# Kernel tuning notes

Measured on AMD Instinct MI355X. Metric: run time of the kernel, lower is better.

The kernel has to match this reference:

```python
import jax, jax.numpy as jnp
import numpy as np

N_ATOMS = 8192
N_BONDS = 8192
N_ANGLES = 16384
N_DIHEDRALS = 24576


def _chain_idx(key, n, arity):
    # base atom index + consecutive offsets -> guaranteed-distinct atoms per interaction
    base = jax.random.randint(key, (n, 1), 0, N_ATOMS - arity, dtype=jnp.int32)
    return base + jnp.arange(arity, dtype=jnp.int32)[None, :]


def setup_inputs() -> dict:
    key = jax.random.key(0)
    ks = jax.random.split(key, 12)
    positions = jax.random.normal(ks[0], (N_ATOMS, 3), dtype=jnp.float32) * 3.0
    # LJ pair params: strictly-upper-triangular like the original __init__ loops
    triu = jnp.triu(jnp.ones((N_ATOMS, N_ATOMS), dtype=jnp.float32), k=1)
    sigma = jax.random.uniform(ks[1], (N_ATOMS, N_ATOMS), dtype=jnp.float32) * triu
    epsilon = jax.random.uniform(ks[2], (N_ATOMS, N_ATOMS), dtype=jnp.float32) * 0.2 * triu
    bond_idx = _chain_idx(ks[3], N_BONDS, 2)
    k_bond = jax.random.uniform(ks[4], (N_BONDS,), dtype=jnp.float32) * 300.0 + 100.0
    r0 = jax.random.uniform(ks[5], (N_BONDS,), dtype=jnp.float32) + 1.0
    angle_idx = _chain_idx(ks[6], N_ANGLES, 3)
    k_angle = jax.random.uniform(ks[7], (N_ANGLES,), dtype=jnp.float32) * 50.0 + 10.0
    theta0 = jax.random.uniform(ks[8], (N_ANGLES,), dtype=jnp.float32) * 2.0 + 0.5
    dihedral_idx = _chain_idx(ks[9], N_DIHEDRALS, 4)
    k_dihedral = jax.random.uniform(ks[10], (N_DIHEDRALS,), dtype=jnp.float32) * 5.0
    default_phase = jax.random.uniform(ks[11], (N_DIHEDRALS,), dtype=jnp.float32) * np.pi
    n_mult = jax.random.randint(jax.random.fold_in(key, 99), (N_DIHEDRALS,), 1, 4).astype(jnp.float32)
    return {
        "positions": positions,
        "sigma": sigma,
        "epsilon": epsilon,
        "k_bond": k_bond,
        "r0": r0,
        "bond_idx": bond_idx,
        "k_angle": k_angle,
        "theta0": theta0,
        "angle_idx": angle_idx,
        "k_dihedral": k_dihedral,
        "default_phase": default_phase,
        "n_mult": n_mult,
        "dihedral_idx": dihedral_idx,
    }


def _energy(positions, sigma, epsilon, k_bond, r0, bond_idx,
            k_angle, theta0, angle_idx, k_dihedral, default_phase, n_mult, dihedral_idx):
    # pairwise distance map (cdist) + 1e-9, as in get_distance_map
    sq = jnp.sum(positions * positions, axis=-1)  # [N]
    d2 = sq[:, None] + sq[None, :] - 2.0 * (positions @ positions.T)
    dist = jnp.sqrt(jnp.maximum(d2, 0.0)) + 1e-9  # [N, N]

    # bonds: gather pair distances, harmonic energy
    bd = dist[bond_idx[:, 0], bond_idx[:, 1]]
    bond_e = jnp.sum(0.5 * k_bond * (bd - r0) ** 2)

    # angles: acos of normalized dot product
    p1 = positions[angle_idx[:, 0]]
    p2 = positions[angle_idx[:, 1]]
    p3 = positions[angle_idx[:, 2]]
    v1 = p2 - p1
    v2 = p2 - p3
    cos_a = jnp.sum(v1 * v2, axis=-1) / (
        jnp.linalg.norm(v1, axis=1) * jnp.linalg.norm(v2, axis=1))
    ang = jnp.arccos(cos_a)
    angle_e = jnp.sum(0.5 * k_angle * (ang - theta0) ** 2)

    # dihedrals (faithful to the original formulas, including its denominators)
    q1 = positions[dihedral_idx[:, 0]]
    q2 = positions[dihedral_idx[:, 1]]
    q3 = positions[dihedral_idx[:, 2]]
    q4 = positions[dihedral_idx[:, 3]]
    w1 = q2 - q1
    w2 = q3 - q2
    w3 = q4 - q3
    n1 = jnp.cross(w1, w2)
    n2 = jnp.cross(w2, w3)
    cos_d = jnp.sum(n1 * n2, axis=-1) / (
        jnp.linalg.norm(w1, axis=1) * jnp.linalg.norm(w2, axis=1))
    sin_d = jnp.sum(jnp.cross(n1, n2) * w2, axis=-1) / (
        jnp.linalg.norm(w2, axis=1) * jnp.linalg.norm(n1, axis=1) * jnp.linalg.norm(n2, axis=1))
    dih = jnp.arctan2(sin_d, cos_d)
    dihedral_e = jnp.sum(0.5 * k_dihedral * (1.0 + jnp.cos(n_mult * dih - default_phase)))

    # Lennard-Jones over dense NxN pair matrices
    r6 = (sigma / dist) ** 6
    r12 = r6 * r6
    lj_e = jnp.sum(4.0 * epsilon * (r12 - r6))

    # NOTE: original forward computes coulomb but does NOT add it to total_energy
    return bond_e + angle_e + dihedral_e + lj_e


def reference(positions, sigma, epsilon, k_bond, r0, bond_idx,
              k_angle, theta0, angle_idx, k_dihedral, default_phase, n_mult, dihedral_idx):
    return _energy(positions, sigma, epsilon, k_bond, r0, bond_idx,
                   k_angle, theta0, angle_idx, k_dihedral, default_phase, n_mult, dihedral_idx)
```

## Files before the change

kernel.cpp:

```cpp
#include <hip/hip_runtime.h>

#define NATOMS   8192
#define NVEC     (NATOMS / 4)
#define BT       256
#define NB_LJ    NATOMS
#define NBONDS   8192
#define NANGLES  16384
#define NDIH     24576
#define NB_BOND  ((NBONDS + NANGLES + NDIH) / BT)

__device__ __forceinline__ float sq_np(float x, float y, float z)
{
    return __fadd_rn(__fadd_rn(__fmul_rn(x, x), __fmul_rn(y, y)),
                     __fmul_rn(z, z));
}

__global__ __launch_bounds__(BT)
void lj_kernel(const float* __restrict__ pos,
               const float* __restrict__ sigma,
               const float* __restrict__ eps,
               float* __restrict__ partial)
{
    const int i   = blockIdx.x;
    const int tid = threadIdx.x;

    const float xi = pos[3 * i + 0];
    const float yi = pos[3 * i + 1];
    const float zi = pos[3 * i + 2];
    const float sqi = sq_np(xi, yi, zi);

    const float* __restrict__ srow = sigma + (size_t)i * NATOMS;
    const float* __restrict__ erow = eps   + (size_t)i * NATOMS;

    float acc = 0.0f;
    const int v0 = (i + 1) >> 2;

    for (int v = v0 + tid; v < NVEC; v += BT) {
        const float4 s4 = *reinterpret_cast<const float4*>(srow + 4 * v);
        const float4 e4 = *reinterpret_cast<const float4*>(erow + 4 * v);
        const float4 p0 = *reinterpret_cast<const float4*>(pos + 12 * v + 0);
        const float4 p1 = *reinterpret_cast<const float4*>(pos + 12 * v + 4);
        const float4 p2 = *reinterpret_cast<const float4*>(pos + 12 * v + 8);

        const float px[4] = { p0.x, p0.w, p1.z, p2.y };
        const float py[4] = { p0.y, p1.x, p1.w, p2.z };
        const float pz[4] = { p0.z, p1.y, p2.x, p2.w };
        const float ss[4] = { s4.x, s4.y, s4.z, s4.w };
        const float ee[4] = { e4.x, e4.y, e4.z, e4.w };

        #pragma unroll
        for (int k = 0; k < 4; ++k) {
            float t = __fmul_rn(xi, px[k]);
            t = fmaf(yi, py[k], t);
            t = fmaf(zi, pz[k], t);
            const float sqj = sq_np(px[k], py[k], pz[k]);
            const float d2  = __fsub_rn(__fadd_rn(sqi, sqj),
                                        __fmul_rn(2.0f, t));
            const float dist  = __fadd_rn(__fsqrt_rn(fmaxf(d2, 0.0f)), 1e-9f);
            const float ratio = __fdiv_rn(ss[k], dist);
            const float r2  = __fmul_rn(ratio, ratio);
            const float r6  = __fmul_rn(__fmul_rn(r2, r2), r2);
            const float r12 = __fmul_rn(r6, r6);
            acc += 4.0f * ee[k] * (r12 - r6);
        }
    }

    #pragma unroll
    for (int off = 32; off > 0; off >>= 1)
        acc += __shfl_down(acc, off, 64);
    __shared__ float red[BT / 64];
    if ((tid & 63) == 0) red[tid >> 6] = acc;
    __syncthreads();
    if (tid == 0)
        partial[i] = red[0] + red[1] + red[2] + red[3];
}

__global__ __launch_bounds__(BT)
void bonded_kernel(const float* __restrict__ pos,
                   const float* __restrict__ k_bond,
                   const float* __restrict__ r0,
                   const int*   __restrict__ bidx,
                   const float* __restrict__ k_angle,
                   const float* __restrict__ th0,
                   const int*   __restrict__ aidx,
                   const float* __restrict__ k_dih,
                   const float* __restrict__ phase,
                   const float* __restrict__ nmult,
                   const int*   __restrict__ didx,
                   float* __restrict__ partial)
{
    const int t = blockIdx.x * BT + threadIdx.x;
    float e = 0.0f;

    if (t < NBONDS) {
        const int a = bidx[2 * t + 0];
        const int b = bidx[2 * t + 1];
        const float xa = pos[3 * a + 0], ya = pos[3 * a + 1], za = pos[3 * a + 2];
        const float xb = pos[3 * b + 0], yb = pos[3 * b + 1], zb = pos[3 * b + 2];
        float dt2 = __fmul_rn(xa, xb);
        dt2 = fmaf(ya, yb, dt2);
        dt2 = fmaf(za, zb, dt2);
        const float d2 = __fsub_rn(__fadd_rn(sq_np(xa, ya, za), sq_np(xb, yb, zb)),
                                   __fmul_rn(2.0f, dt2));
        const float d  = __fadd_rn(__fsqrt_rn(fmaxf(d2, 0.0f)), 1e-9f);
        const float dd = d - r0[t];
        e = 0.5f * k_bond[t] * dd * dd;
    } else if (t < NBONDS + NANGLES) {
        const int u = t - NBONDS;
        const int a = aidx[3 * u + 0];
        const int b = aidx[3 * u + 1];
        const int c = aidx[3 * u + 2];
        const float v1x = pos[3 * b + 0] - pos[3 * a + 0];
        const float v1y = pos[3 * b + 1] - pos[3 * a + 1];
        const float v1z = pos[3 * b + 2] - pos[3 * a + 2];
        const float v2x = pos[3 * b + 0] - pos[3 * c + 0];
        const float v2y = pos[3 * b + 1] - pos[3 * c + 1];
        const float v2z = pos[3 * b + 2] - pos[3 * c + 2];
        const float dot = fmaf(v1x, v2x, fmaf(v1y, v2y, v1z * v2z));
        const float n1  = sqrtf(fmaf(v1x, v1x, fmaf(v1y, v1y, v1z * v1z)));
        const float n2  = sqrtf(fmaf(v2x, v2x, fmaf(v2y, v2y, v2z * v2z)));
        float ca = dot / (n1 * n2);
        ca = fminf(1.0f, fmaxf(-1.0f, ca));
        const float ang = acosf(ca);
        const float dth = ang - th0[u];
        e = 0.5f * k_angle[u] * dth * dth;
    } else {
        const int u = t - NBONDS - NANGLES;
        const int a = didx[4 * u + 0];
        const int b = didx[4 * u + 1];
        const int c = didx[4 * u + 2];
        const int d = didx[4 * u + 3];
        const float w1x = pos[3 * b + 0] - pos[3 * a + 0];
        const float w1y = pos[3 * b + 1] - pos[3 * a + 1];
        const float w1z = pos[3 * b + 2] - pos[3 * a + 2];
        const float w2x = pos[3 * c + 0] - pos[3 * b + 0];
        const float w2y = pos[3 * c + 1] - pos[3 * b + 1];
        const float w2z = pos[3 * c + 2] - pos[3 * b + 2];
        const float w3x = pos[3 * d + 0] - pos[3 * c + 0];
        const float w3y = pos[3 * d + 1] - pos[3 * c + 1];
        const float w3z = pos[3 * d + 2] - pos[3 * c + 2];
        const float n1x = w1y * w2z - w1z * w2y;
        const float n1y = w1z * w2x - w1x * w2z;
        const float n1z = w1x * w2y - w1y * w2x;
        const float n2x = w2y * w3z - w2z * w3y;
        const float n2y = w2z * w3x - w2x * w3z;
        const float n2z = w2x * w3y - w2y * w3x;
        const float dot12 = fmaf(n1x, n2x, fmaf(n1y, n2y, n1z * n2z));
        const float nw1 = sqrtf(fmaf(w1x, w1x, fmaf(w1y, w1y, w1z * w1z)));
        const float nw2 = sqrtf(fmaf(w2x, w2x, fmaf(w2y, w2y, w2z * w2z)));
        const float nn1 = sqrtf(fmaf(n1x, n1x, fmaf(n1y, n1y, n1z * n1z)));
        const float nn2 = sqrtf(fmaf(n2x, n2x, fmaf(n2y, n2y, n2z * n2z)));
        const float cos_d = dot12 / (nw1 * nw2);
        const float cx = n1y * n2z - n1z * n2y;
        const float cy = n1z * n2x - n1x * n2z;
        const float cz = n1x * n2y - n1y * n2x;
        const float sden = nw2 * nn1 * nn2;
        const float sin_d = fmaf(cx, w2x, fmaf(cy, w2y, cz * w2z)) / sden;
        const float dih = atan2f(sin_d, cos_d);
        e = 0.5f * k_dih[u] * (1.0f + cosf(nmult[u] * dih - phase[u]));
    }

    #pragma unroll
    for (int off = 32; off > 0; off >>= 1)
        e += __shfl_down(e, off, 64);
    __shared__ float red[BT / 64];
    if ((threadIdx.x & 63) == 0) red[threadIdx.x >> 6] = e;
    __syncthreads();
    if (threadIdx.x == 0)
        partial[blockIdx.x] = red[0] + red[1] + red[2] + red[3];
}

__global__ __launch_bounds__(BT)
void reduce_kernel(const float* __restrict__ partial, int n,
                   float* __restrict__ out)
{
    double s = 0.0;
    for (int i = threadIdx.x; i < n; i += BT)
        s += (double)partial[i];
    #pragma unroll
    for (int off = 32; off > 0; off >>= 1)
        s += __shfl_down(s, off, 64);
    __shared__ double red[BT / 64];
    if ((threadIdx.x & 63) == 0) red[threadIdx.x >> 6] = s;
    __syncthreads();
    if (threadIdx.x == 0)
        out[0] = (float)(red[0] + red[1] + red[2] + red[3]);
}

extern "C" void kernel_launch(void* const* d_in, const int* in_sizes, int n_in,
                              void* d_out, int out_size, void* d_ws, size_t ws_size,
                              hipStream_t stream)
{
    const float* pos   = (const float*)d_in[0];
    const float* sigma = (const float*)d_in[1];
    const float* eps   = (const float*)d_in[2];
    const float* kb    = (const float*)d_in[3];
    const float* r0    = (const float*)d_in[4];
    const int*   bidx  = (const int*)  d_in[5];
    const float* ka    = (const float*)d_in[6];
    const float* th0   = (const float*)d_in[7];
    const int*   aidx  = (const int*)  d_in[8];
    const float* kd    = (const float*)d_in[9];
    const float* ph    = (const float*)d_in[10];
    const float* nm    = (const float*)d_in[11];
    const int*   didx  = (const int*)  d_in[12];

    float* ws  = (float*)d_ws;
    float* out = (float*)d_out;

    lj_kernel<<<NB_LJ, BT, 0, stream>>>(pos, sigma, eps, ws);
    bonded_kernel<<<NB_BOND, BT, 0, stream>>>(pos, kb, r0, bidx, ka, th0, aidx,
                                              kd, ph, nm, didx, ws + NB_LJ);
    reduce_kernel<<<1, BT, 0, stream>>>(ws, NB_LJ + NB_BOND, out);
}
```

Baseline: 58.02 us.

## Fuse LJ and bonded kernels, pair triangular rows, precompute SoA positions

Adds a pre-pass that writes positions as separate x/y/z arrays plus squared norms, so the LJ inner loop uses aligned vector loads and skips recomputing norms. Each LJ block now handles rows i and N-1-i, which evens out the triangular work, and the bonded terms are folded into the same launch. Sigma and epsilon are read with nontemporal loads so the streaming matrices do not evict the reused position data from cache. The final reduce uses 1024 threads, and the extra launch adds some fixed overhead.

```diff
diff --git a/kernel.cpp b/kernel.cpp
--- a/kernel.cpp
+++ b/kernel.cpp
@@ -3,11 +3,20 @@
 #define NATOMS   8192
 #define NVEC     (NATOMS / 4)
 #define BT       256
-#define NB_LJ    NATOMS
+#define NB_PAIR  (NATOMS / 2)
 #define NBONDS   8192
 #define NANGLES  16384
 #define NDIH     24576
 #define NB_BOND  ((NBONDS + NANGLES + NDIH) / BT)
+#define NB_MAIN  (NB_PAIR + NB_BOND)
+
+typedef float floatx4 __attribute__((ext_vector_type(4)));
+
+#define WS_PX 0
+#define WS_PY NATOMS
+#define WS_PZ (2 * NATOMS)
+#define WS_SQ (3 * NATOMS)
+#define WS_PARTIAL (4 * NATOMS)
 
 __device__ __forceinline__ float sq_np(float x, float y, float z)
 {
@@ -16,175 +25,193 @@
 }
 
 __global__ __launch_bounds__(BT)
-void lj_kernel(const float* __restrict__ pos,
-               const float* __restrict__ sigma,
-               const float* __restrict__ eps,
-               float* __restrict__ partial)
-{
-    const int i   = blockIdx.x;
-    const int tid = threadIdx.x;
-
-    const float xi = pos[3 * i + 0];
-    const float yi = pos[3 * i + 1];
-    const float zi = pos[3 * i + 2];
-    const float sqi = sq_np(xi, yi, zi);
+void soa_kernel(const float* __restrict__ pos, float* __restrict__ ws)
+{
+    const int i = blockIdx.x * BT + threadIdx.x;
+    if (i < NATOMS) {
+        const float x = pos[3 * i + 0];
+        const float y = pos[3 * i + 1];
+        const float z = pos[3 * i + 2];
+        ws[WS_PX + i] = x;
+        ws[WS_PY + i] = y;
+        ws[WS_PZ + i] = z;
+        ws[WS_SQ + i] = sq_np(x, y, z);
+    }
+}
+
+__device__ __forceinline__ float lj_row(const float* __restrict__ sigma,
+                                        const float* __restrict__ eps,
+                                        const float* __restrict__ ws,
+                                        int i, int tid)
+{
+    const float xi  = ws[WS_PX + i];
+    const float yi  = ws[WS_PY + i];
+    const float zi  = ws[WS_PZ + i];
+    const float sqi = ws[WS_SQ + i];
 
     const float* __restrict__ srow = sigma + (size_t)i * NATOMS;
     const float* __restrict__ erow = eps   + (size_t)i * NATOMS;
+    const float* __restrict__ pxp  = ws + WS_PX;
+    const float* __restrict__ pyp  = ws + WS_PY;
+    const float* __restrict__ pzp  = ws + WS_PZ;
+    const float* __restrict__ sqp  = ws + WS_SQ;
 
     float acc = 0.0f;
     const int v0 = (i + 1) >> 2;
 
+    #pragma unroll 2
     for (int v = v0 + tid; v < NVEC; v += BT) {
-        const float4 s4 = *reinterpret_cast<const float4*>(srow + 4 * v);
-        const float4 e4 = *reinterpret_cast<const float4*>(erow + 4 * v);
-        const float4 p0 = *reinterpret_cast<const float4*>(pos + 12 * v + 0);
-        const float4 p1 = *reinterpret_cast<const float4*>(pos + 12 * v + 4);
-        const float4 p2 = *reinterpret_cast<const float4*>(pos + 12 * v + 8);
-
-        const float px[4] = { p0.x, p0.w, p1.z, p2.y };
-        const float py[4] = { p0.y, p1.x, p1.w, p2.z };
-        const float pz[4] = { p0.z, p1.y, p2.x, p2.w };
-        const float ss[4] = { s4.x, s4.y, s4.z, s4.w };
-        const float ee[4] = { e4.x, e4.y, e4.z, e4.w };
+        const floatx4 s4 = __builtin_nontemporal_load(
+            reinterpret_cast<const floatx4*>(srow + 4 * v));
+        const floatx4 e4 = __builtin_nontemporal_load(
+            reinterpret_cast<const floatx4*>(erow + 4 * v));
+        const floatx4 px4 = *reinterpret_cast<const floatx4*>(pxp + 4 * v);
+        const floatx4 py4 = *reinterpret_cast<const floatx4*>(pyp + 4 * v);
+        const floatx4 pz4 = *reinterpret_cast<const floatx4*>(pzp + 4 * v);
+        const floatx4 sq4 = *reinterpret_cast<const floatx4*>(sqp + 4 * v);
 
         #pragma unroll
         for (int k = 0; k < 4; ++k) {
-            float t = __fmul_rn(xi, px[k]);
-            t = fmaf(yi, py[k], t);
-            t = fmaf(zi, pz[k], t);
-            const float sqj = sq_np(px[k], py[k], pz[k]);
-            const float d2  = __fsub_rn(__fadd_rn(sqi, sqj),
-                                        __fmul_rn(2.0f, t));
+            float t = __fmul_rn(xi, px4[k]);
+            t = fmaf(yi, py4[k], t);
+            t = fmaf(zi, pz4[k], t);
+            const float d2 = __fsub_rn(__fadd_rn(sqi, sq4[k]),
+                                       __fmul_rn(2.0f, t));
             const float dist  = __fadd_rn(__fsqrt_rn(fmaxf(d2, 0.0f)), 1e-9f);
-            const float ratio = __fdiv_rn(ss[k], dist);
+            const float ratio = __fdiv_rn(s4[k], dist);
             const float r2  = __fmul_rn(ratio, ratio);
             const float r6  = __fmul_rn(__fmul_rn(r2, r2), r2);
             const float r12 = __fmul_rn(r6, r6);
-            acc += 4.0f * ee[k] * (r12 - r6);
+            acc += 4.0f * e4[k] * (r12 - r6);
         }
     }
-
-    #pragma unroll
-    for (int off = 32; off > 0; off >>= 1)
-        acc += __shfl_down(acc, off, 64);
-    __shared__ float red[BT / 64];
-    if ((tid & 63) == 0) red[tid >> 6] = acc;
-    __syncthreads();
-    if (tid == 0)
-        partial[i] = red[0] + red[1] + red[2] + red[3];
+    return acc;
 }
 
 __global__ __launch_bounds__(BT)
-void bonded_kernel(const float* __restrict__ pos,
-                   const float* __restrict__ k_bond,
-                   const float* __restrict__ r0,
-                   const int*   __restrict__ bidx,
-                   const float* __restrict__ k_angle,
-                   const float* __restrict__ th0,
-                   const int*   __restrict__ aidx,
-                   const float* __restrict__ k_dih,
-                   const float* __restrict__ phase,
-                   const float* __restrict__ nmult,
-                   const int*   __restrict__ didx,
-                   float* __restrict__ partial)
-{
-    const int t = blockIdx.x * BT + threadIdx.x;
+void main_kernel(const float* __restrict__ sigma,
+                 const float* __restrict__ eps,
+                 const float* __restrict__ pos,
+                 const float* __restrict__ k_bond,
+                 const float* __restrict__ r0,
+                 const int*   __restrict__ bidx,
+                 const float* __restrict__ k_angle,
+                 const float* __restrict__ th0,
+                 const int*   __restrict__ aidx,
+                 const float* __restrict__ k_dih,
+                 const float* __restrict__ phase,
+                 const float* __restrict__ nmult,
+                 const int*   __restrict__ didx,
+                 float* __restrict__ ws)
+{
+    const int bid = blockIdx.x;
+    const int tid = threadIdx.x;
     float e = 0.0f;
 
-    if (t < NBONDS) {
-        const int a = bidx[2 * t + 0];
-        const int b = bidx[2 * t + 1];
-        const float xa = pos[3 * a + 0], ya = pos[3 * a + 1], za = pos[3 * a + 2];
-        const float xb = pos[3 * b + 0], yb = pos[3 * b + 1], zb = pos[3 * b + 2];
-        float dt2 = __fmul_rn(xa, xb);
-        dt2 = fmaf(ya, yb, dt2);
-        dt2 = fmaf(za, zb, dt2);
-        const float d2 = __fsub_rn(__fadd_rn(sq_np(xa, ya, za), sq_np(xb, yb, zb)),
-                                   __fmul_rn(2.0f, dt2));
-        const float d  = __fadd_rn(__fsqrt_rn(fmaxf(d2, 0.0f)), 1e-9f);
-        const float dd = d - r0[t];
-        e = 0.5f * k_bond[t] * dd * dd;
-    } else if (t < NBONDS + NANGLES) {
-        const int u = t - NBONDS;
-        const int a = aidx[3 * u + 0];
-        const int b = aidx[3 * u + 1];
-        const int c = aidx[3 * u + 2];
-        const float v1x = pos[3 * b + 0] - pos[3 * a + 0];
-        const float v1y = pos[3 * b + 1] - pos[3 * a + 1];
-        const float v1z = pos[3 * b + 2] - pos[3 * a + 2];
-        const float v2x = pos[3 * b + 0] - pos[3 * c + 0];
-        const float v2y = pos[3 * b + 1] - pos[3 * c + 1];
-        const float v2z = pos[3 * b + 2] - pos[3 * c + 2];
-        const float dot = fmaf(v1x, v2x, fmaf(v1y, v2y, v1z * v2z));
-        const float n1  = sqrtf(fmaf(v1x, v1x, fmaf(v1y, v1y, v1z * v1z)));
-        const float n2  = sqrtf(fmaf(v2x, v2x, fmaf(v2y, v2y, v2z * v2z)));
-        float ca = dot / (n1 * n2);
-        ca = fminf(1.0f, fmaxf(-1.0f, ca));
-        const float ang = acosf(ca);
-        const float dth = ang - th0[u];
-        e = 0.5f * k_angle[u] * dth * dth;
+    if (bid < NB_PAIR) {
+        e  = lj_row(sigma, eps, ws, bid, tid);
+        e += lj_row(sigma, eps, ws, NATOMS - 1 - bid, tid);
     } else {
-        const int u = t - NBONDS - NANGLES;
-        const int a = didx[4 * u + 0];
-        const int b = didx[4 * u + 1];
-        const int c = didx[4 * u + 2];
-        const int d = didx[4 * u + 3];
-        const float w1x = pos[3 * b + 0] - pos[3 * a + 0];
-        const float w1y = pos[3 * b + 1] - pos[3 * a + 1];
-        const float w1z = pos[3 * b + 2] - pos[3 * a + 2];
-        const float w2x = pos[3 * c + 0] - pos[3 * b + 0];
-        const float w2y = pos[3 * c + 1] - pos[3 * b + 1];
-        const float w2z = pos[3 * c + 2] - pos[3 * b + 2];
-        const float w3x = pos[3 * d + 0] - pos[3 * c + 0];
-        const float w3y = pos[3 * d + 1] - pos[3 * c + 1];
-        const float w3z = pos[3 * d + 2] - pos[3 * c + 2];
-        const float n1x = w1y * w2z - w1z * w2y;
-        const float n1y = w1z * w2x - w1x * w2z;
-        const float n1z = w1x * w2y - w1y * w2x;
-        const float n2x = w2y * w3z - w2z * w3y;
-        const float n2y = w2z * w3x - w2x * w3z;
-        const float n2z = w2x * w3y - w2y * w3x;
-        const float dot12 = fmaf(n1x, n2x, fmaf(n1y, n2y, n1z * n2z));
-        const float nw1 = sqrtf(fmaf(w1x, w1x, fmaf(w1y, w1y, w1z * w1z)));
-        const float nw2 = sqrtf(fmaf(w2x, w2x, fmaf(w2y, w2y, w2z * w2z)));
-        const float nn1 = sqrtf(fmaf(n1x, n1x, fmaf(n1y, n1y, n1z * n1z)));
-        const float nn2 = sqrtf(fmaf(n2x, n2x, fmaf(n2y, n2y, n2z * n2z)));
-        const float cos_d = dot12 / (nw1 * nw2);
-        const float cx = n1y * n2z - n1z * n2y;
-        const float cy = n1z * n2x - n1x * n2z;
-        const float cz = n1x * n2y - n1y * n2x;
-        const float sden = nw2 * nn1 * nn2;
-        const float sin_d = fmaf(cx, w2x, fmaf(cy, w2y, cz * w2z)) / sden;
-        const float dih = atan2f(sin_d, cos_d);
-        e = 0.5f * k_dih[u] * (1.0f + cosf(nmult[u] * dih - phase[u]));
+        const int t = (bid - NB_PAIR) * BT + tid;
+        if (t < NBONDS) {
+            const int a = bidx[2 * t + 0];
+            const int b = bidx[2 * t + 1];
+            const float xa = pos[3 * a + 0], ya = pos[3 * a + 1], za = pos[3 * a + 2];
+            const float xb = pos[3 * b + 0], yb = pos[3 * b + 1], zb = pos[3 * b + 2];
+            float dt2 = __fmul_rn(xa, xb);
+            dt2 = fmaf(ya, yb, dt2);
+            dt2 = fmaf(za, zb, dt2);
+            const float d2 = __fsub_rn(__fadd_rn(sq_np(xa, ya, za), sq_np(xb, yb, zb)),
+                                       __fmul_rn(2.0f, dt2));
+            const float d  = __fadd_rn(__fsqrt_rn(fmaxf(d2, 0.0f)), 1e-9f);
+            const float dd = d - r0[t];
+            e = 0.5f * k_bond[t] * dd * dd;
+        } else if (t < NBONDS + NANGLES) {
+            const int u = t - NBONDS;
+            const int a = aidx[3 * u + 0];
+            const int b = aidx[3 * u + 1];
+            const int c = aidx[3 * u + 2];
+            const float v1x = pos[3 * b + 0] - pos[3 * a + 0];
+            const float v1y = pos[3 * b + 1] - pos[3 * a + 1];
+            const float v1z = pos[3 * b + 2] - pos[3 * a + 2];
+            const float v2x = pos[3 * b + 0] - pos[3 * c + 0];
+            const float v2y = pos[3 * b + 1] - pos[3 * c + 1];
+            const float v2z = pos[3 * b + 2] - pos[3 * c + 2];
+            const float dot = fmaf(v1x, v2x, fmaf(v1y, v2y, v1z * v2z));
+            const float n1  = sqrtf(fmaf(v1x, v1x, fmaf(v1y, v1y, v1z * v1z)));
+            const float n2  = sqrtf(fmaf(v2x, v2x, fmaf(v2y, v2y, v2z * v2z)));
+            float ca = dot / (n1 * n2);
+            ca = fminf(1.0f, fmaxf(-1.0f, ca));
+            const float ang = acosf(ca);
+            const float dth = ang - th0[u];
+            e = 0.5f * k_angle[u] * dth * dth;
+        } else {
+            const int u = t - NBONDS - NANGLES;
+            const int a = didx[4 * u + 0];
+            const int b = didx[4 * u + 1];
+            const int c = didx[4 * u + 2];
+            const int d = didx[4 * u + 3];
+            const float w1x = pos[3 * b + 0] - pos[3 * a + 0];
+            const float w1y = pos[3 * b + 1] - pos[3 * a + 1];
+            const float w1z = pos[3 * b + 2] - pos[3 * a + 2];
+            const float w2x = pos[3 * c + 0] - pos[3 * b + 0];
+            const float w2y = pos[3 * c + 1] - pos[3 * b + 1];
+            const float w2z = pos[3 * c + 2] - pos[3 * b + 2];
+            const float w3x = pos[3 * d + 0] - pos[3 * c + 0];
+            const float w3y = pos[3 * d + 1] - pos[3 * c + 1];
+            const float w3z = pos[3 * d + 2] - pos[3 * c + 2];
+            const float n1x = w1y * w2z - w1z * w2y;
+            const float n1y = w1z * w2x - w1x * w2z;
+            const float n1z = w1x * w2y - w1y * w2x;
+            const float n2x = w2y * w3z - w2z * w3y;
+            const float n2y = w2z * w3x - w2x * w3z;
+            const float n2z = w2x * w3y - w2y * w3x;
+            const float dot12 = fmaf(n1x, n2x, fmaf(n1y, n2y, n1z * n2z));
+            const float nw1 = sqrtf(fmaf(w1x, w1x, fmaf(w1y, w1y, w1z * w1z)));
+            const float nw2 = sqrtf(fmaf(w2x, w2x, fmaf(w2y, w2y, w2z * w2z)));
+            const float nn1 = sqrtf(fmaf(n1x, n1x, fmaf(n1y, n1y, n1z * n1z)));
+            const float nn2 = sqrtf(fmaf(n2x, n2x, fmaf(n2y, n2y, n2z * n2z)));
+            const float cos_d = dot12 / (nw1 * nw2);
+            const float cx = n1y * n2z - n1z * n2y;
+            const float cy = n1z * n2x - n1x * n2z;
+            const float cz = n1x * n2y - n1y * n2x;
+            const float sden = nw2 * nn1 * nn2;
+            const float sin_d = fmaf(cx, w2x, fmaf(cy, w2y, cz * w2z)) / sden;
+            const float dih = atan2f(sin_d, cos_d);
+            e = 0.5f * k_dih[u] * (1.0f + cosf(nmult[u] * dih - phase[u]));
+        }
     }
 
     #pragma unroll
     for (int off = 32; off > 0; off >>= 1)
         e += __shfl_down(e, off, 64);
     __shared__ float red[BT / 64];
-    if ((threadIdx.x & 63) == 0) red[threadIdx.x >> 6] = e;
+    if ((tid & 63) == 0) red[tid >> 6] = e;
     __syncthreads();
-    if (threadIdx.x == 0)
-        partial[blockIdx.x] = red[0] + red[1] + red[2] + red[3];
-}
-
-__global__ __launch_bounds__(BT)
+    if (tid == 0)
+        ws[WS_PARTIAL + bid] = red[0] + red[1] + red[2] + red[3];
+}
+
+#define RT 1024
+__global__ __launch_bounds__(RT)
 void reduce_kernel(const float* __restrict__ partial, int n,
                    float* __restrict__ out)
 {
     double s = 0.0;
-    for (int i = threadIdx.x; i < n; i += BT)
+    for (int i = threadIdx.x; i < n; i += RT)
         s += (double)partial[i];
     #pragma unroll
     for (int off = 32; off > 0; off >>= 1)
         s += __shfl_down(s, off, 64);
-    __shared__ double red[BT / 64];
+    __shared__ double red[RT / 64];
     if ((threadIdx.x & 63) == 0) red[threadIdx.x >> 6] = s;
     __syncthreads();
-    if (threadIdx.x == 0)
-        out[0] = (float)(red[0] + red[1] + red[2] + red[3]);
+    if (threadIdx.x == 0) {
+        double t = 0.0;
+        #pragma unroll
+        for (int w = 0; w < RT / 64; ++w) t += red[w];
+        out[0] = (float)t;
+    }
 }
 
 extern "C" void kernel_launch(void* const* d_in, const int* in_sizes, int n_in,
@@ -208,8 +235,8 @@
     float* ws  = (float*)d_ws;
     float* out = (float*)d_out;
 
-    lj_kernel<<<NB_LJ, BT, 0, stream>>>(pos, sigma, eps, ws);
-    bonded_kernel<<<NB_BOND, BT, 0, stream>>>(pos, kb, r0, bidx, ka, th0, aidx,
-                                              kd, ph, nm, didx, ws + NB_LJ);
-    reduce_kernel<<<1, BT, 0, stream>>>(ws, NB_LJ + NB_BOND, out);
-}
+    soa_kernel<<<NATOMS / BT, BT, 0, stream>>>(pos, ws);
+    main_kernel<<<NB_MAIN, BT, 0, stream>>>(sigma, eps, pos, kb, r0, bidx,
+                                            ka, th0, aidx, kd, ph, nm, didx, ws);
+    reduce_kernel<<<1, RT, 0, stream>>>(ws + WS_PARTIAL, NB_MAIN, out);
+}
```

Result: slower. 77.90 us (+34.3%).
